# Performance work log

Measured on AMD Instinct MI355X. Metric: run time of the kernel, lower is better.

## Reference

```python
import jax, jax.numpy as jnp
import numpy as np

C_IN = 256
C_RED = max(4, C_IN // 4)  # 64


def setup_inputs() -> dict:
    key = jax.random.key(0)
    k1, k2, k3, k4, k5 = jax.random.split(key, 5)
    B, C, H, W = 4, C_IN, 64, 64
    x = jax.random.normal(k1, (B, C, H, W), dtype=jnp.float32)
    # 1x1 convs (no bias) are just channel matmuls: weight shape (out_ch, in_ch)
    s_in = 1.0 / np.sqrt(C)
    s_red = 1.0 / np.sqrt(C_RED)
    Wq = jax.random.normal(k2, (C_RED, C), dtype=jnp.float32) * s_in
    Wk = jax.random.normal(k3, (C_RED, C), dtype=jnp.float32) * s_in
    Wv = jax.random.normal(k4, (C_RED, C), dtype=jnp.float32) * s_in
    Wp = jax.random.normal(k5, (C, C_RED), dtype=jnp.float32) * s_red
    return {"x": x, "Wq": Wq, "Wk": Wk, "Wv": Wv, "Wp": Wp}


def reference(x, Wq, Wk, Wv, Wp):
    B, C, H, W = x.shape
    N = H * W
    xf = x.reshape(B, C, N)                       # (B, C, N)
    q = jnp.einsum('rc,bcn->bnr', Wq, xf)         # (B, N, c_red)
    k = jnp.einsum('rc,bcn->brn', Wk, xf)         # (B, c_red, N)
    v = jnp.einsum('rc,bcn->bnr', Wv, xf)         # (B, N, c_red)
    scale = 1.0 / jnp.sqrt(jnp.float32(k.shape[1]))
    attn = jnp.einsum('bnr,brm->bnm', q, k) * scale   # (B, N, N)
    attn = jax.nn.softmax(attn, axis=-1)
    out = jnp.einsum('bnm,bmr->brn', attn, v)     # (B, c_red, N)
    out = jnp.einsum('cr,brn->bcn', Wp, out)      # (B, C, N)
    return out.reshape(B, C, H, W) + x
```

## Files before the change

### kernel.cpp

```cpp
#include <hip/hip_runtime.h>
#include <hip/hip_bf16.h>

#define CIN 256
#define CRED 64
#define NB 4
#define NN 4096

typedef float v4f __attribute__((ext_vector_type(4)));
typedef short v8s __attribute__((ext_vector_type(8)));
typedef unsigned short u16;
typedef u16 u16x4 __attribute__((ext_vector_type(4)));
typedef u16 u16x8 __attribute__((ext_vector_type(8)));
typedef unsigned int u32;

#define LOG2E 1.4426950408889634f

__device__ __forceinline__ u16 f2bf(float f) {
    union { float f; u32 u; } v; v.f = f;
    u32 r = (v.u + 0x7FFFu + ((v.u >> 16) & 1u)) >> 16;
    return (u16)r;
}
__device__ __forceinline__ float bf2f(u16 s) {
    union { u32 u; float f; } v; v.u = ((u32)s) << 16;
    return v.f;
}
__device__ __forceinline__ u32 pkbf(float a, float b) {
    float2 f; f.x = a; f.y = b;
    __hip_bfloat162 h = __float22bfloat162_rn(f);
    union { __hip_bfloat162 h; u32 u; } c; c.h = h;
    return c.u;
}
__device__ __forceinline__ v4f mfma16(v8s a, v8s b, v4f c) {
    return __builtin_amdgcn_mfma_f32_16x16x32_bf16(a, b, c, 0, 0, 0);
}
__device__ __forceinline__ float fexp2(float x) {
#if __has_builtin(__builtin_amdgcn_exp2f)
    return __builtin_amdgcn_exp2f(x);
#else
    return exp2f(x);
#endif
}

__global__ __launch_bounds__(256) void k_wconv(const float* __restrict__ Wq,
                                               const float* __restrict__ Wk,
                                               const float* __restrict__ Wv,
                                               u16* __restrict__ Wb) {
    int t = threadIdx.x;
    int idx = (blockIdx.x * 256 + t) * 4;
    int row = idx >> 8;
    int mat = row >> 6, r = row & 63, col = idx & 255;
    const float* src = (mat == 0) ? Wq : (mat == 1) ? Wk : Wv;
    float4 v = *(const float4*)&src[r * 256 + col];
    float s = (mat == 0) ? (0.125f * LOG2E) : 1.0f;
    u16x4 o;
    o[0] = f2bf(v.x * s); o[1] = f2bf(v.y * s);
    o[2] = f2bf(v.z * s); o[3] = f2bf(v.w * s);
    *(u16x4*)&Wb[idx] = o;
}

__global__ __launch_bounds__(256) void k_qkvm(const float* __restrict__ x,
                                              const u16* __restrict__ Wb,
                                              u16* __restrict__ Q, u16* __restrict__ K,
                                              u16* __restrict__ V) {
    int t = threadIdx.x;
    int wv = t >> 6, lane = t & 63, c15 = lane & 15, quad = lane >> 4;
    int n0g = blockIdx.x * 32;
    int b = n0g >> 12, nb = n0g & 4095;
    const float* xb = x + ((size_t)b << 20);

    v8s Af[2][8];
#pragma unroll
    for (int nt = 0; nt < 2; ++nt) {
        const float* px = xb + nb + nt * 16 + c15 + (size_t)quad * 8 * 4096;
#pragma unroll
        for (int kc = 0; kc < 8; ++kc) {
            float f[8];
#pragma unroll
            for (int j = 0; j < 8; ++j)
                f[j] = px[((size_t)kc * 32 + j) * 4096];
            union { v8s s; u32 w[4]; } pk;
            pk.w[0] = pkbf(f[0], f[1]); pk.w[1] = pkbf(f[2], f[3]);
            pk.w[2] = pkbf(f[4], f[5]); pk.w[3] = pkbf(f[6], f[7]);
            Af[nt][kc] = pk.s;
        }
    }

#pragma unroll
    for (int rti = 0; rti < 3; ++rti) {
        int rt = wv * 3 + rti;
        const u16* wrow = Wb + (size_t)(rt * 16 + c15) * 256 + quad * 8;
        v8s Bf[8];
#pragma unroll
        for (int kc = 0; kc < 8; ++kc) Bf[kc] = *(const v8s*)&wrow[kc * 32];
#pragma unroll
        for (int nt = 0; nt < 2; ++nt) {
            v4f acc = {0.f, 0.f, 0.f, 0.f};
#pragma unroll
            for (int kc = 0; kc < 8; ++kc)
                acc = mfma16(Af[nt][kc], Bf[kc], acc);
            if (rt < 8) {
                u16* base = (rt < 4) ? Q : K;
                u16* dst = base + ((size_t)b << 18)
                         + (size_t)(nb + nt * 16 + quad * 4) * 64
                         + (rt & 3) * 16 + c15;
#pragma unroll
                for (int g = 0; g < 4; ++g) dst[g * 64] = f2bf(acc[g]);
            } else {
                int hi2 = ((nb + nt * 16) >> 4) & 3;
                size_t base = ((size_t)b * 64 + (rt - 8) * 16 + c15) * 4096
                            + (size_t)((nb + nt * 16) & ~63) + hi2;
#pragma unroll
                for (int g = 0; g < 4; ++g)
                    V[base + (quad * 4 + g) * 4] = f2bf(acc[g]);
            }
        }
    }
}

__global__ __launch_bounds__(256, 3) void k_flash(const u16* __restrict__ Q,
                                                  const u16* __restrict__ K,
                                                  const u16* __restrict__ V,
                                                  u16* __restrict__ OP,
                                                  float* __restrict__ Lb,
                                                  int sh) {
    __shared__ __align__(16) u16 KV[2][2][4096];
    __shared__ __align__(16) u16 Pl[4][32][72];
    int t = threadIdx.x;
    int p = blockIdx.x & ((1u << sh) - 1);
    int tile = blockIdx.x >> sh;
    int b = tile >> 5;
    int n0 = (tile & 31) * 128;
    int wv = t >> 6;
    int lane = t & 63;
    int c15 = lane & 15;
    int quad = lane >> 4;
    int nw = n0 + wv * 32;
    const u16* Qb = Q + ((size_t)b << 18);
    const u16* Kb = K + ((size_t)b << 18);
    const u16* Vb = V + ((size_t)b << 18);

    v8s Qa[2][2];
#pragma unroll
    for (int rg = 0; rg < 2; ++rg)
#pragma unroll
        for (int c2 = 0; c2 < 2; ++c2)
            Qa[rg][c2] = *(const v8s*)&Qb[(size_t)(nw + rg * 16 + c15) * 64 + c2 * 32 + quad * 8];

    v4f O[2][4];
    float ls[2][4];
#pragma unroll
    for (int rg = 0; rg < 2; ++rg)
#pragma unroll
        for (int g = 0; g < 4; ++g) {
            ls[rg][g] = 0.f;
#pragma unroll
            for (int cg = 0; cg < 4; ++cg) O[rg][cg][g] = 0.f;
        }

    int mlen = NN >> sh;
    int m0 = p * mlen;
    int iters = mlen >> 6;

    int lrow = lane >> 3;
    int cs16 = (((lane & 7) ^ lrow) << 3);
    const u16* gK = Kb + ((size_t)(wv * 16 + lrow) << 6) + cs16;
    const u16* gV = Vb + ((size_t)(wv * 16 + lrow) << 12) + cs16;

    auto stage = [&](int buf, int mt) {
#pragma unroll
        for (int i = 0; i < 2; ++i) {
            __builtin_amdgcn_global_load_lds(
                (const __attribute__((address_space(1))) void*)(gK + ((size_t)(mt + i * 8) << 6)),
                (__attribute__((address_space(3))) void*)&KV[buf][0][(wv * 2 + i) << 9],
                16, 0, 0);
            __builtin_amdgcn_global_load_lds(
                (const __attribute__((address_space(1))) void*)(gV + ((size_t)i << 15) + mt),
                (__attribute__((address_space(3))) void*)&KV[buf][1][(wv * 2 + i) << 9],
                16, 0, 0);
        }
    };

    int swz = (c15 & 7) << 4;
    int col0 = (quad << 4) ^ swz;
    int col1 = col0 ^ 64;
    int rbase = c15 << 7;

    stage(0, m0);
    __syncthreads();

    for (int it = 0; it < iters; ++it) {
        int cur = it & 1;
        if (it + 1 < iters) stage(cur ^ 1, m0 + (it + 1) * 64);
        const char* KB = (const char*)&KV[cur][0][0];
        const char* VB = (const char*)&KV[cur][1][0];

        v4f S[2][4];
#pragma unroll
        for (int rg = 0; rg < 2; ++rg)
#pragma unroll
            for (int s = 0; s < 4; ++s)
#pragma unroll
                for (int g = 0; g < 4; ++g) S[rg][s][g] = 0.f;

        __builtin_amdgcn_s_setprio(1);
#pragma unroll
        for (int s = 0; s < 4; ++s) {
            v8s kb0 = *(const v8s*)(KB + rbase + s * 2048 + col0);
            v8s kb1 = *(const v8s*)(KB + rbase + s * 2048 + col1);
            S[0][s] = mfma16(Qa[0][0], kb0, S[0][s]);
            S[1][s] = mfma16(Qa[1][0], kb0, S[1][s]);
            S[0][s] = mfma16(Qa[0][1], kb1, S[0][s]);
            S[1][s] = mfma16(Qa[1][1], kb1, S[1][s]);
        }
        __builtin_amdgcn_s_setprio(0);

#pragma unroll
        for (int rg = 0; rg < 2; ++rg) {
            float E[4][4];
#pragma unroll
            for (int s = 0; s < 4; ++s)
#pragma unroll
                for (int g = 0; g < 4; ++g) {
                    float e = fexp2(S[rg][s][g]);
                    E[s][g] = e;
                    ls[rg][g] += e;
                }
#pragma unroll
            for (int g = 0; g < 4; ++g) {
                union { u16x4 v; u32 w[2]; } p2;
                p2.w[0] = pkbf(E[0][g], E[1][g]);
                p2.w[1] = pkbf(E[2][g], E[3][g]);
                *(u16x4*)&Pl[wv][rg * 16 + quad * 4 + g][c15 * 4] = p2.v;
            }
        }

        v8s Pa[2][2];
#pragma unroll
        for (int rg = 0; rg < 2; ++rg)
#pragma unroll
            for (int c2 = 0; c2 < 2; ++c2)
                Pa[rg][c2] = *(const v8s*)&Pl[wv][rg * 16 + c15][c2 * 32 + quad * 8];

        __builtin_amdgcn_s_setprio(1);
#pragma unroll
        for (int cg = 0; cg < 4; ++cg) {
            v8s vb0 = *(const v8s*)(VB + (cg << 11) + rbase + col0);
            v8s vb1 = *(const v8s*)(VB + (cg << 11) + rbase + col1);
            O[0][cg] = mfma16(Pa[0][0], vb0, O[0][cg]);
            O[1][cg] = mfma16(Pa[1][0], vb0, O[1][cg]);
            O[0][cg] = mfma16(Pa[0][1], vb1, O[0][cg]);
            O[1][cg] = mfma16(Pa[1][1], vb1, O[1][cg]);
        }
        __builtin_amdgcn_s_setprio(0);
        __syncthreads();
    }

    u16* OPp = OP + (size_t)p * (NB * NN * 64) + (size_t)b * NN * 64;
#pragma unroll
    for (int rg = 0; rg < 2; ++rg)
#pragma unroll
        for (int cg = 0; cg < 4; ++cg)
#pragma unroll
            for (int g = 0; g < 4; ++g) {
                int n = nw + rg * 16 + quad * 4 + g;
                OPp[(size_t)n * 64 + cg * 16 + c15] = f2bf(O[rg][cg][g]);
            }
#pragma unroll
    for (int rg = 0; rg < 2; ++rg)
#pragma unroll
        for (int g = 0; g < 4; ++g) {
            float v = ls[rg][g];
#pragma unroll
            for (int off = 1; off <= 8; off <<= 1) v += __shfl_xor(v, off);
            ls[rg][g] = v;
        }
    if (c15 == 0) {
        float* Lp = Lb + (size_t)p * (NB * NN) + (size_t)b * NN;
#pragma unroll
        for (int rg = 0; rg < 2; ++rg)
#pragma unroll
            for (int g = 0; g < 4; ++g) {
                int n = nw + rg * 16 + quad * 4 + g;
                Lp[n] = ls[rg][g];
            }
    }
}

#define OMP 72
template <int NSP>
__global__ __launch_bounds__(256) void k_proj(const u16* __restrict__ OP,
                                              const float* __restrict__ Lb,
                                              const float* __restrict__ Wp,
                                              const float* __restrict__ x,
                                              float* __restrict__ out) {
    __shared__ __align__(16) u16 Om[32 * OMP];
    int t = threadIdx.x;
    int b = blockIdx.x >> 7;
    int n0 = (blockIdx.x & 127) * 32;

    {
        int n_l = t >> 3, r0 = (t & 7) * 8;
        size_t nidx = (size_t)b * NN + n0 + n_l;
        float o[8] = {0.f, 0.f, 0.f, 0.f, 0.f, 0.f, 0.f, 0.f};
        float l = 0.f;
#pragma unroll
        for (int p = 0; p < NSP; ++p) {
            u16x8 u = *(const u16x8*)&OP[((size_t)p * (NB * NN) + nidx) * 64 + r0];
#pragma unroll
            for (int j = 0; j < 8; ++j) o[j] += bf2f(u[j]);
            l += Lb[(size_t)p * (NB * NN) + nidx];
        }
        float inv = 1.0f / l;
        union { u16x8 v; u32 w[4]; } p2;
        p2.w[0] = pkbf(o[0] * inv, o[1] * inv);
        p2.w[1] = pkbf(o[2] * inv, o[3] * inv);
        p2.w[2] = pkbf(o[4] * inv, o[5] * inv);
        p2.w[3] = pkbf(o[6] * inv, o[7] * inv);
        *(u16x8*)&Om[n_l * OMP + r0] = p2.v;
    }
    __syncthreads();

    int lane = t & 63, wvv = t >> 6, c15 = lane & 15, quad = lane >> 4;
    v8s Bf[2][2];
#pragma unroll
    for (int nt = 0; nt < 2; ++nt) {
        Bf[nt][0] = *(const v8s*)&Om[(nt * 16 + c15) * OMP + quad * 8];
        Bf[nt][1] = *(const v8s*)&Om[(nt * 16 + c15) * OMP + 32 + quad * 8];
    }
#pragma unroll
    for (int ct0 = 0; ct0 < 4; ++ct0) {
        int ct = wvv * 4 + ct0;
        const float* wrow = Wp + (size_t)(ct * 16 + c15) * 64 + quad * 8;
        float4 wa = *(const float4*)&wrow[0];
        float4 wb = *(const float4*)&wrow[4];
        float4 wc = *(const float4*)&wrow[32];
        float4 wd = *(const float4*)&wrow[36];
        union { v8s s; u32 w[4]; } A0, A1;
        A0.w[0] = pkbf(wa.x, wa.y); A0.w[1] = pkbf(wa.z, wa.w);
        A0.w[2] = pkbf(wb.x, wb.y); A0.w[3] = pkbf(wb.z, wb.w);
        A1.w[0] = pkbf(wc.x, wc.y); A1.w[1] = pkbf(wc.z, wc.w);
        A1.w[2] = pkbf(wd.x, wd.y); A1.w[3] = pkbf(wd.z, wd.w);
#pragma unroll
        for (int nt = 0; nt < 2; ++nt) {
            v4f acc = {0.f, 0.f, 0.f, 0.f};
            acc = mfma16(A0.s, Bf[nt][0], acc);
            acc = mfma16(A1.s, Bf[nt][1], acc);
            size_t base = ((size_t)(b * 256 + ct * 16 + quad * 4)) * 4096 + n0 + nt * 16 + c15;
#pragma unroll
            for (int g = 0; g < 4; ++g)
                out[base + (size_t)g * 4096] = acc[g] + x[base + (size_t)g * 4096];
        }
    }
}

extern "C" void kernel_launch(void* const* d_in, const int* in_sizes, int n_in,
                              void* d_out, int out_size, void* d_ws, size_t ws_size,
                              hipStream_t stream) {
    const float* x  = (const float*)d_in[0];
    const float* Wq = (const float*)d_in[1];
    const float* Wk = (const float*)d_in[2];
    const float* Wv = (const float*)d_in[3];
    const float* Wp = (const float*)d_in[4];
    float* out = (float*)d_out;
    char* ws = (char*)d_ws;

    int nsp = (ws_size >= (size_t)24 * 1024 * 1024) ? 8 : 4;
    int sh = (nsp == 8) ? 3 : 2;

    u16* Wb  = (u16*)(ws);
    u16* Q   = (u16*)(ws + 262144);
    u16* K   = (u16*)(ws + 262144 + 2097152);
    u16* V   = (u16*)(ws + 262144 + 2 * 2097152);
    u16* OP  = (u16*)(ws + 262144 + 3 * 2097152);
    float* Lbuf = (float*)(ws + 262144 + (size_t)(3 + nsp) * 2097152);

    k_wconv<<<48, 256, 0, stream>>>(Wq, Wk, Wv, Wb);
    k_qkvm<<<512, 256, 0, stream>>>(x, Wb, Q, K, V);
    k_flash<<<NB * 32 * nsp, 256, 0, stream>>>(Q, K, V, OP, Lbuf, sh);
    if (nsp == 8)
        k_proj<8><<<NB * 128, 256, 0, stream>>>(OP, Lbuf, Wp, x, out);
    else
        k_proj<4><<<NB * 128, 256, 0, stream>>>(OP, Lbuf, Wp, x, out);
}
```

Baseline: 122.7 us.

## Compute softmax row sums with MFMA, stage x via LDS, fix split count

The attention kernel now gets the softmax denominator from extra MFMA instructions that multiply the bf16 probability tiles by a ones vector. This replaces the per-element VALU accumulation and the final cross-lane shuffle reduction. Note the sums now come from bf16-rounded probabilities. The QKV projection kernel loads x with coalesced float4 reads, converts it to bf16 and transposes it through shared memory, replacing strided scalar global loads. The key-split count is also fixed at 4 instead of choosing 8 when the workspace is large enough.

```diff
diff --git a/kernel.cpp b/kernel.cpp
--- a/kernel.cpp
+++ b/kernel.cpp
@@ -62,28 +62,38 @@
                                               const u16* __restrict__ Wb,
                                               u16* __restrict__ Q, u16* __restrict__ K,
                                               u16* __restrict__ V) {
+    __shared__ __align__(16) u16 Xl[1056 * 8];
     int t = threadIdx.x;
     int wv = t >> 6, lane = t & 63, c15 = lane & 15, quad = lane >> 4;
     int n0g = blockIdx.x * 32;
     int b = n0g >> 12, nb = n0g & 4095;
     const float* xb = x + ((size_t)b << 20);
 
+    {
+        int cb = t >> 3, n4 = (t & 7) * 4;
+        const float* px = xb + (size_t)(cb * 8) * 4096 + nb + n4;
+        float4 f[8];
+#pragma unroll
+        for (int j = 0; j < 8; ++j)
+            f[j] = *(const float4*)&px[(size_t)j * 4096];
+#pragma unroll
+        for (int i = 0; i < 4; ++i) {
+            union { u16x8 v; u32 w[4]; } pk;
+            pk.w[0] = pkbf(((const float*)&f[0])[i], ((const float*)&f[1])[i]);
+            pk.w[1] = pkbf(((const float*)&f[2])[i], ((const float*)&f[3])[i]);
+            pk.w[2] = pkbf(((const float*)&f[4])[i], ((const float*)&f[5])[i]);
+            pk.w[3] = pkbf(((const float*)&f[6])[i], ((const float*)&f[7])[i]);
+            *(u16x8*)&Xl[(size_t)(cb * 33 + n4 + i) * 8] = pk.v;
+        }
+    }
+    __syncthreads();
+
     v8s Af[2][8];
 #pragma unroll
-    for (int nt = 0; nt < 2; ++nt) {
-        const float* px = xb + nb + nt * 16 + c15 + (size_t)quad * 8 * 4096;
-#pragma unroll
-        for (int kc = 0; kc < 8; ++kc) {
-            float f[8];
-#pragma unroll
-            for (int j = 0; j < 8; ++j)
-                f[j] = px[((size_t)kc * 32 + j) * 4096];
-            union { v8s s; u32 w[4]; } pk;
-            pk.w[0] = pkbf(f[0], f[1]); pk.w[1] = pkbf(f[2], f[3]);
-            pk.w[2] = pkbf(f[4], f[5]); pk.w[3] = pkbf(f[6], f[7]);
-            Af[nt][kc] = pk.s;
-        }
-    }
+    for (int nt = 0; nt < 2; ++nt)
+#pragma unroll
+        for (int kc = 0; kc < 8; ++kc)
+            Af[nt][kc] = *(const v8s*)&Xl[(size_t)((kc * 4 + quad) * 33 + nt * 16 + c15) * 8];
 
 #pragma unroll
     for (int rti = 0; rti < 3; ++rti) {
@@ -146,16 +156,21 @@
         for (int c2 = 0; c2 < 2; ++c2)
             Qa[rg][c2] = *(const v8s*)&Qb[(size_t)(nw + rg * 16 + c15) * 64 + c2 * 32 + quad * 8];
 
+    union { u16x8 u; v8s s; } on;
+#pragma unroll
+    for (int j = 0; j < 8; ++j) on.u[j] = 0x3F80;
+
     v4f O[2][4];
-    float ls[2][4];
-#pragma unroll
-    for (int rg = 0; rg < 2; ++rg)
+    v4f Lacc[2];
+#pragma unroll
+    for (int rg = 0; rg < 2; ++rg) {
 #pragma unroll
         for (int g = 0; g < 4; ++g) {
-            ls[rg][g] = 0.f;
+            Lacc[rg][g] = 0.f;
 #pragma unroll
             for (int cg = 0; cg < 4; ++cg) O[rg][cg][g] = 0.f;
         }
+    }
 
     int mlen = NN >> sh;
     int m0 = p * mlen;
@@ -216,20 +231,15 @@
 
 #pragma unroll
         for (int rg = 0; rg < 2; ++rg) {
-            float E[4][4];
-#pragma unroll
-            for (int s = 0; s < 4; ++s)
-#pragma unroll
-                for (int g = 0; g < 4; ++g) {
-                    float e = fexp2(S[rg][s][g]);
-                    E[s][g] = e;
-                    ls[rg][g] += e;
-                }
 #pragma unroll
             for (int g = 0; g < 4; ++g) {
+                float e0 = fexp2(S[rg][0][g]);
+                float e1 = fexp2(S[rg][1][g]);
+                float e2 = fexp2(S[rg][2][g]);
+                float e3 = fexp2(S[rg][3][g]);
                 union { u16x4 v; u32 w[2]; } p2;
-                p2.w[0] = pkbf(E[0][g], E[1][g]);
-                p2.w[1] = pkbf(E[2][g], E[3][g]);
+                p2.w[0] = pkbf(e0, e1);
+                p2.w[1] = pkbf(e2, e3);
                 *(u16x4*)&Pl[wv][rg * 16 + quad * 4 + g][c15 * 4] = p2.v;
             }
         }
@@ -251,6 +261,10 @@
             O[0][cg] = mfma16(Pa[0][1], vb1, O[0][cg]);
             O[1][cg] = mfma16(Pa[1][1], vb1, O[1][cg]);
         }
+        Lacc[0] = mfma16(Pa[0][0], on.s, Lacc[0]);
+        Lacc[0] = mfma16(Pa[0][1], on.s, Lacc[0]);
+        Lacc[1] = mfma16(Pa[1][0], on.s, Lacc[1]);
+        Lacc[1] = mfma16(Pa[1][1], on.s, Lacc[1]);
         __builtin_amdgcn_s_setprio(0);
         __syncthreads();
     }
@@ -265,15 +279,6 @@
                 int n = nw + rg * 16 + quad * 4 + g;
                 OPp[(size_t)n * 64 + cg * 16 + c15] = f2bf(O[rg][cg][g]);
             }
-#pragma unroll
-    for (int rg = 0; rg < 2; ++rg)
-#pragma unroll
-        for (int g = 0; g < 4; ++g) {
-            float v = ls[rg][g];
-#pragma unroll
-            for (int off = 1; off <= 8; off <<= 1) v += __shfl_xor(v, off);
-            ls[rg][g] = v;
-        }
     if (c15 == 0) {
         float* Lp = Lb + (size_t)p * (NB * NN) + (size_t)b * NN;
 #pragma unroll
@@ -281,7 +286,7 @@
 #pragma unroll
             for (int g = 0; g < 4; ++g) {
                 int n = nw + rg * 16 + quad * 4 + g;
-                Lp[n] = ls[rg][g];
+                Lp[n] = Lacc[rg][g];
             }
     }
 }
@@ -364,8 +369,8 @@
     float* out = (float*)d_out;
     char* ws = (char*)d_ws;
 
-    int nsp = (ws_size >= (size_t)24 * 1024 * 1024) ? 8 : 4;
-    int sh = (nsp == 8) ? 3 : 2;
+    const int nsp = 4;
+    const int sh = 2;
 
     u16* Wb  = (u16*)(ws);
     u16* Q   = (u16*)(ws + 262144);
@@ -377,8 +382,5 @@
     k_wconv<<<48, 256, 0, stream>>>(Wq, Wk, Wv, Wb);
     k_qkvm<<<512, 256, 0, stream>>>(x, Wb, Q, K, V);
     k_flash<<<NB * 32 * nsp, 256, 0, stream>>>(Q, K, V, OP, Lbuf, sh);
-    if (nsp == 8)
-        k_proj<8><<<NB * 128, 256, 0, stream>>>(OP, Lbuf, Wp, x, out);
-    else
-        k_proj<4><<<NB * 128, 256, 0, stream>>>(OP, Lbuf, Wp, x, out);
-}
+    k_proj<4><<<NB * 128, 256, 0, stream>>>(OP, Lbuf, Wp, x, out);
+}
```

Result: faster. 117.8 us (-4.0%).
